# Kernel optimization log

Measured on AMD Instinct MI355X. Metric: run time of the kernel, lower is better.

## Reference

```python
import jax, jax.numpy as jnp
import numpy as np

TOP_K = 2

def setup_inputs() -> dict:
    key = jax.random.key(0)
    k1, k2, k3, k4 = jax.random.split(key, 4)
    T, H, E, I = 2048, 1024, 16, 768
    x = jax.random.normal(k1, (T, H), dtype=jnp.float32)
    gate_w = jax.random.normal(k2, (E, H), dtype=jnp.float32) * 0.02
    w13 = jax.random.normal(k3, (E, 2 * I, H), dtype=jnp.float32) * 0.02
    w2 = jax.random.normal(k4, (E, H, I), dtype=jnp.float32) * 0.02
    return {"x": x, "gate_w": gate_w, "w13": w13, "w2": w2}


def reference(x, gate_w, w13, w2):
    # x: [T, H] tokens; gate_w: [E, H]; w13: [E, 2I, H]; w2: [E, H, I]
    T, H = x.shape
    E = gate_w.shape[0]
    I = w2.shape[-1]

    # --- route: gate matmul + softmax top-k router (renormalize=True) ---
    router_logits = x @ gate_w.T                                  # [T, E]
    probs = jax.nn.softmax(router_logits.astype(jnp.float32), axis=-1)
    topk_w, topk_ids = jax.lax.top_k(probs, TOP_K)                # [T, K]
    topk_w = topk_w / jnp.sum(topk_w, axis=-1, keepdims=True)     # renormalize
    topk_w = topk_w.astype(x.dtype)

    # dense combine weights [T, E]: scatter top-k weights back (dispatch/combine)
    dense_gates = jnp.zeros((T, E), dtype=x.dtype)
    dense_gates = dense_gates.at[jnp.arange(T)[:, None], topk_ids].add(topk_w)

    # --- apply sparse experts: SwiGLU FFN per expert, combined by gates ---
    def expert_step(acc, packed):
        w13_e, w2_e, g_e = packed        # [2I,H], [H,I], [T]
        h = x @ w13_e.T                  # [T, 2I]
        act = jax.nn.silu(h[:, :I]) * h[:, I:]   # gate_proj * up_proj
        return acc + g_e[:, None] * (act @ w2_e.T), None

    acc0 = jnp.zeros_like(x)
    out, _ = jax.lax.scan(expert_step, acc0, (w13, w2, dense_gates.T))
    return out
```

## Files before the change

### kernel.cpp

```cpp
#include <hip/hip_runtime.h>
#include <hip/hip_bf16.h>
#include <hip/hip_fp16.h>
#include <math.h>

#define T_TOK 2048
#define HDIM  1024
#define NEXP  16
#define IDIM  768
#define BM    32
#define MAXROWS 4608

using f16   = _Float16;
using f16x4 = __attribute__((ext_vector_type(4))) _Float16;
using f16x8 = __attribute__((ext_vector_type(8))) _Float16;
using f32x4 = __attribute__((ext_vector_type(4))) float;

__global__ __launch_bounds__(256) void router_kernel(
    const float* __restrict__ x, const float* __restrict__ gw,
    int* __restrict__ tok_e, float* __restrict__ tok_w, int* __restrict__ cnt)
{
    int wave = threadIdx.x >> 6;
    int lane = threadIdx.x & 63;
    int t = blockIdx.x * 4 + wave;
    if (t >= T_TOK) return;

    const float* xrow = x + (size_t)t * HDIM;
    float xv[16];
#pragma unroll
    for (int j = 0; j < 16; ++j) xv[j] = xrow[lane + 64 * j];

    float logits[NEXP];
#pragma unroll
    for (int e = 0; e < NEXP; ++e) {
        const float* gr = gw + (size_t)e * HDIM;
        float s = 0.f;
#pragma unroll
        for (int j = 0; j < 16; ++j) s += xv[j] * gr[lane + 64 * j];
#pragma unroll
        for (int o = 32; o > 0; o >>= 1) s += __shfl_xor(s, o, 64);
        logits[e] = s;
    }

    int i1 = 0; float m1 = logits[0];
#pragma unroll
    for (int e = 1; e < NEXP; ++e) if (logits[e] > m1) { m1 = logits[e]; i1 = e; }
    int i2 = -1; float m2 = -3.0e38f;
#pragma unroll
    for (int e = 0; e < NEXP; ++e) if (e != i1 && logits[e] > m2) { m2 = logits[e]; i2 = e; }

    float w1 = 1.f / (1.f + expf(m2 - m1));
    float w2 = 1.f - w1;

    if (lane == 0) {
        tok_e[t * 2 + 0] = i1; tok_e[t * 2 + 1] = i2;
        tok_w[t * 2 + 0] = w1; tok_w[t * 2 + 1] = w2;
        atomicAdd(&cnt[i1], 1);
        atomicAdd(&cnt[i2], 1);
    }
}

__global__ void prefix_kernel(const int* __restrict__ cnt, int* __restrict__ base,
                              int* __restrict__ total)
{
    if (threadIdx.x == 0) {
        int b = 0;
        for (int e = 0; e < NEXP; ++e) {
            base[e] = b;
            b += (cnt[e] + BM - 1) & ~(BM - 1);
        }
        base[NEXP] = b;
        *total = b;
    }
}

__global__ __launch_bounds__(256) void scatter_kernel(
    const int* __restrict__ tok_e, const float* __restrict__ tok_w,
    const int* __restrict__ base, int* __restrict__ cnt2,
    int* __restrict__ rowslot, float* __restrict__ rowgate)
{
    int t = blockIdx.x * 256 + threadIdx.x;
    if (t >= T_TOK) return;
#pragma unroll
    for (int k = 0; k < 2; ++k) {
        int e = tok_e[t * 2 + k];
        int pos = atomicAdd(&cnt2[e], 1);
        int row = base[e] + pos;
        rowslot[row] = t * 2 + k;
        rowgate[row] = tok_w[t * 2 + k];
    }
}

__global__ __launch_bounds__(256) void gemm1_kernel(
    const float* __restrict__ x, const float* __restrict__ w13,
    const int* __restrict__ rowslot, const int* __restrict__ base,
    const int* __restrict__ cnt, const int* __restrict__ total,
    f16* __restrict__ act)
{
    int row0 = blockIdx.x * BM;
    if (row0 >= *total) return;
    int nt = blockIdx.y;

    int e = 0;
#pragma unroll
    for (int i = 1; i < NEXP; ++i) if (base[i] <= row0) e = i;
    int basee = base[e], cnte = cnt[e];

    __shared__ f16  a_sm[32 * 40];
    __shared__ f16  b_sm[128 * 40];
    __shared__ float h_sm[32 * 132];

    int tid = threadIdx.x;

    int ar = tid >> 3, ac = (tid & 7) * 4;
    bool avalid = (row0 + ar - basee) < cnte;
    const float* aptr = x;
    if (avalid) {
        int tok = rowslot[row0 + ar] >> 1;
        aptr = x + (size_t)tok * HDIM + ac;
    }

    int br = tid >> 1, bc = (tid & 1) * 16;
    int wrow = (br < 64) ? (nt * 64 + br) : (IDIM + nt * 64 + (br - 64));
    const float* bptr = w13 + (size_t)e * 2 * IDIM * HDIM + (size_t)wrow * HDIM + bc;

    int wv = tid >> 6, lane = tid & 63, l16 = lane & 15, lk = lane >> 4;
    f32x4 acc[2][2] = {};

    for (int k0 = 0; k0 < HDIM; k0 += 32) {
        __syncthreads();
        float4 av = avalid ? *(const float4*)(aptr + k0) : float4{0.f, 0.f, 0.f, 0.f};
        f16x4 a4; a4[0] = (f16)av.x; a4[1] = (f16)av.y; a4[2] = (f16)av.z; a4[3] = (f16)av.w;
        *(f16x4*)&a_sm[ar * 40 + ac] = a4;
#pragma unroll
        for (int i = 0; i < 4; ++i) {
            float4 bv = *(const float4*)(bptr + k0 + i * 4);
            f16x4 b4; b4[0] = (f16)bv.x; b4[1] = (f16)bv.y; b4[2] = (f16)bv.z; b4[3] = (f16)bv.w;
            *(f16x4*)&b_sm[br * 40 + bc + i * 4] = b4;
        }
        __syncthreads();

        f16x8 af0 = *(const f16x8*)&a_sm[(l16) * 40 + lk * 8];
        f16x8 af1 = *(const f16x8*)&a_sm[(16 + l16) * 40 + lk * 8];
        f16x8 bf0 = *(const f16x8*)&b_sm[(wv * 32 + l16) * 40 + lk * 8];
        f16x8 bf1 = *(const f16x8*)&b_sm[(wv * 32 + 16 + l16) * 40 + lk * 8];
        acc[0][0] = __builtin_amdgcn_mfma_f32_16x16x32_f16(af0, bf0, acc[0][0], 0, 0, 0);
        acc[0][1] = __builtin_amdgcn_mfma_f32_16x16x32_f16(af0, bf1, acc[0][1], 0, 0, 0);
        acc[1][0] = __builtin_amdgcn_mfma_f32_16x16x32_f16(af1, bf0, acc[1][0], 0, 0, 0);
        acc[1][1] = __builtin_amdgcn_mfma_f32_16x16x32_f16(af1, bf1, acc[1][1], 0, 0, 0);
    }

    __syncthreads();
#pragma unroll
    for (int mh = 0; mh < 2; ++mh)
#pragma unroll
        for (int nh = 0; nh < 2; ++nh)
#pragma unroll
            for (int j = 0; j < 4; ++j)
                h_sm[(mh * 16 + lk * 4 + j) * 132 + wv * 32 + nh * 16 + l16] = acc[mh][nh][j];
    __syncthreads();

    int rr = tid >> 3, cc = (tid & 7) * 8;
    f16x8 o;
#pragma unroll
    for (int i = 0; i < 8; ++i) {
        float hg = h_sm[rr * 132 + cc + i];
        float hu = h_sm[rr * 132 + 64 + cc + i];
        float s = hg / (1.f + expf(-hg));
        o[i] = (f16)(s * hu);
    }
    *(f16x8*)&act[(size_t)(row0 + rr) * IDIM + nt * 64 + cc] = o;
}

__global__ __launch_bounds__(256) void gemm2_kernel(
    const f16* __restrict__ act, const float* __restrict__ w2,
    const int* __restrict__ rowslot, const float* __restrict__ rowgate,
    const int* __restrict__ base, const int* __restrict__ cnt, const int* __restrict__ total,
    float* __restrict__ out)
{
    int row0 = blockIdx.x * BM;
    if (row0 >= *total) return;
    int nt = blockIdx.y;

    int e = 0;
#pragma unroll
    for (int i = 1; i < NEXP; ++i) if (base[i] <= row0) e = i;
    int basee = base[e], cnte = cnt[e];

    __shared__ f16 a_sm[32 * 40];
    __shared__ f16 b_sm[128 * 40];

    int tid = threadIdx.x;
    int ar = tid >> 3, ac = (tid & 7) * 4;
    const f16* aptr = act + (size_t)(row0 + ar) * IDIM + ac;
    int br = tid >> 1, bc = (tid & 1) * 16;
    const float* bptr = w2 + (size_t)e * HDIM * IDIM + (size_t)(nt * 128 + br) * IDIM + bc;

    int wv = tid >> 6, lane = tid & 63, l16 = lane & 15, lk = lane >> 4;
    f32x4 acc[2][2] = {};

    for (int k0 = 0; k0 < IDIM; k0 += 32) {
        __syncthreads();
        *(f16x4*)&a_sm[ar * 40 + ac] = *(const f16x4*)(aptr + k0);
#pragma unroll
        for (int i = 0; i < 4; ++i) {
            float4 bv = *(const float4*)(bptr + k0 + i * 4);
            f16x4 b4; b4[0] = (f16)bv.x; b4[1] = (f16)bv.y; b4[2] = (f16)bv.z; b4[3] = (f16)bv.w;
            *(f16x4*)&b_sm[br * 40 + bc + i * 4] = b4;
        }
        __syncthreads();

        f16x8 af0 = *(const f16x8*)&a_sm[(l16) * 40 + lk * 8];
        f16x8 af1 = *(const f16x8*)&a_sm[(16 + l16) * 40 + lk * 8];
        f16x8 bf0 = *(const f16x8*)&b_sm[(wv * 32 + l16) * 40 + lk * 8];
        f16x8 bf1 = *(const f16x8*)&b_sm[(wv * 32 + 16 + l16) * 40 + lk * 8];
        acc[0][0] = __builtin_amdgcn_mfma_f32_16x16x32_f16(af0, bf0, acc[0][0], 0, 0, 0);
        acc[0][1] = __builtin_amdgcn_mfma_f32_16x16x32_f16(af0, bf1, acc[0][1], 0, 0, 0);
        acc[1][0] = __builtin_amdgcn_mfma_f32_16x16x32_f16(af1, bf0, acc[1][0], 0, 0, 0);
        acc[1][1] = __builtin_amdgcn_mfma_f32_16x16x32_f16(af1, bf1, acc[1][1], 0, 0, 0);
    }

    int colbase = nt * 128 + wv * 32;
#pragma unroll
    for (int mh = 0; mh < 2; ++mh) {
#pragma unroll
        for (int j = 0; j < 4; ++j) {
            int r = mh * 16 + lk * 4 + j;
            int row = row0 + r;
            if ((row - basee) < cnte) {
                int s = rowslot[row];
                float g = rowgate[row];
                float* orow = out + (size_t)(s >> 1) * HDIM + colbase;
                atomicAdd(&orow[l16], g * acc[mh][0][j]);
                atomicAdd(&orow[16 + l16], g * acc[mh][1][j]);
            }
        }
    }
}

extern "C" void kernel_launch(void* const* d_in, const int* in_sizes, int n_in,
                              void* d_out, int out_size, void* d_ws, size_t ws_size,
                              hipStream_t stream) {
    const float* x   = (const float*)d_in[0];
    const float* gw  = (const float*)d_in[1];
    const float* w13 = (const float*)d_in[2];
    const float* w2  = (const float*)d_in[3];
    float* out = (float*)d_out;

    char* ws = (char*)d_ws;
    size_t off = 0;
    f16* act       = (f16*)(ws + off);   off += (size_t)MAXROWS * IDIM * 2;
    int* rowslot   = (int*)(ws + off);   off += (size_t)MAXROWS * 4;
    float* rowgate = (float*)(ws + off); off += (size_t)MAXROWS * 4;
    int* tok_e     = (int*)(ws + off);   off += (size_t)T_TOK * 2 * 4;
    float* tok_w   = (float*)(ws + off); off += (size_t)T_TOK * 2 * 4;
    int* cnt       = (int*)(ws + off);   off += 64;
    int* cnt2      = (int*)(ws + off);   off += 64;
    int* base      = (int*)(ws + off);   off += 128;
    int* total     = (int*)(ws + off);   off += 64;

    hipMemsetAsync(cnt, 0, 128, stream);
    hipMemsetAsync(out, 0, (size_t)T_TOK * HDIM * 4, stream);

    router_kernel<<<T_TOK / 4, 256, 0, stream>>>(x, gw, tok_e, tok_w, cnt);
    prefix_kernel<<<1, 64, 0, stream>>>(cnt, base, total);
    scatter_kernel<<<T_TOK / 256, 256, 0, stream>>>(tok_e, tok_w, base, cnt2, rowslot, rowgate);

    dim3 g1(MAXROWS / BM, (2 * IDIM) / 128);
    gemm1_kernel<<<g1, 256, 0, stream>>>(x, w13, rowslot, base, cnt, total, act);

    dim3 g2(MAXROWS / BM, HDIM / 128);
    gemm2_kernel<<<g2, 256, 0, stream>>>(act, w2, rowslot, rowgate, base, cnt, total, out);
}
```

Before: 420.8 us.

## Enlarge MoE GEMM row tiles to 128 and fuse SwiGLU from registers

Row tile per block grows from 32 to 128 so each block reuses a 128x32 weight slice across four times more token rows, cutting redundant fp32 weight reads and conversions. Each wave now computes a 32x128 output sub-tile with 16 MFMAs per k-step instead of 4. In gemm1 the shared-memory staging for the SwiGLU epilogue is dropped and the activation is computed directly from accumulators, since gate and up columns sit in the same lane. Larger padding (MAXROWS raised) adds wasted rows per expert, and higher register use may lower occupancy.

Measured after the change: 353.3 us. 16.0% less time.

```diff
diff --git a/kernel.cpp b/kernel.cpp
--- a/kernel.cpp
+++ b/kernel.cpp
@@ -7,13 +7,20 @@
 #define HDIM  1024
 #define NEXP  16
 #define IDIM  768
-#define BM    32
-#define MAXROWS 4608
+#define BM    128
+#define MAXROWS 6144
 
 using f16   = _Float16;
 using f16x4 = __attribute__((ext_vector_type(4))) _Float16;
 using f16x8 = __attribute__((ext_vector_type(8))) _Float16;
 using f32x4 = __attribute__((ext_vector_type(4))) float;
+
+__device__ __forceinline__ f16x8 cvt2(float4 a, float4 b) {
+    f16x8 r;
+    r[0] = (f16)a.x; r[1] = (f16)a.y; r[2] = (f16)a.z; r[3] = (f16)a.w;
+    r[4] = (f16)b.x; r[5] = (f16)b.y; r[6] = (f16)b.z; r[7] = (f16)b.w;
+    return r;
+}
 
 __global__ __launch_bounds__(256) void router_kernel(
     const float* __restrict__ x, const float* __restrict__ gw,
@@ -105,70 +112,73 @@
     for (int i = 1; i < NEXP; ++i) if (base[i] <= row0) e = i;
     int basee = base[e], cnte = cnt[e];
 
-    __shared__ f16  a_sm[32 * 40];
-    __shared__ f16  b_sm[128 * 40];
-    __shared__ float h_sm[32 * 132];
+    __shared__ f16 a_sm[128 * 40];
+    __shared__ f16 b_sm[128 * 40];
 
     int tid = threadIdx.x;
-
-    int ar = tid >> 3, ac = (tid & 7) * 4;
-    bool avalid = (row0 + ar - basee) < cnte;
+    int srow = tid >> 1;
+    int scol = (tid & 1) * 16;
+
+    bool avalid = (unsigned)(row0 + srow - basee) < (unsigned)cnte;
     const float* aptr = x;
     if (avalid) {
-        int tok = rowslot[row0 + ar] >> 1;
-        aptr = x + (size_t)tok * HDIM + ac;
-    }
-
-    int br = tid >> 1, bc = (tid & 1) * 16;
-    int wrow = (br < 64) ? (nt * 64 + br) : (IDIM + nt * 64 + (br - 64));
-    const float* bptr = w13 + (size_t)e * 2 * IDIM * HDIM + (size_t)wrow * HDIM + bc;
+        int tok = rowslot[row0 + srow] >> 1;
+        aptr = x + (size_t)tok * HDIM + scol;
+    }
+
+    int wrow = (srow < 64) ? (nt * 64 + srow) : (IDIM + nt * 64 + (srow - 64));
+    const float* bptr = w13 + (size_t)e * 2 * IDIM * HDIM + (size_t)wrow * HDIM + scol;
 
     int wv = tid >> 6, lane = tid & 63, l16 = lane & 15, lk = lane >> 4;
-    f32x4 acc[2][2] = {};
+    f32x4 acc[2][8] = {};
 
     for (int k0 = 0; k0 < HDIM; k0 += 32) {
         __syncthreads();
-        float4 av = avalid ? *(const float4*)(aptr + k0) : float4{0.f, 0.f, 0.f, 0.f};
-        f16x4 a4; a4[0] = (f16)av.x; a4[1] = (f16)av.y; a4[2] = (f16)av.z; a4[3] = (f16)av.w;
-        *(f16x4*)&a_sm[ar * 40 + ac] = a4;
-#pragma unroll
-        for (int i = 0; i < 4; ++i) {
-            float4 bv = *(const float4*)(bptr + k0 + i * 4);
-            f16x4 b4; b4[0] = (f16)bv.x; b4[1] = (f16)bv.y; b4[2] = (f16)bv.z; b4[3] = (f16)bv.w;
-            *(f16x4*)&b_sm[br * 40 + bc + i * 4] = b4;
-        }
-        __syncthreads();
-
-        f16x8 af0 = *(const f16x8*)&a_sm[(l16) * 40 + lk * 8];
-        f16x8 af1 = *(const f16x8*)&a_sm[(16 + l16) * 40 + lk * 8];
-        f16x8 bf0 = *(const f16x8*)&b_sm[(wv * 32 + l16) * 40 + lk * 8];
-        f16x8 bf1 = *(const f16x8*)&b_sm[(wv * 32 + 16 + l16) * 40 + lk * 8];
-        acc[0][0] = __builtin_amdgcn_mfma_f32_16x16x32_f16(af0, bf0, acc[0][0], 0, 0, 0);
-        acc[0][1] = __builtin_amdgcn_mfma_f32_16x16x32_f16(af0, bf1, acc[0][1], 0, 0, 0);
-        acc[1][0] = __builtin_amdgcn_mfma_f32_16x16x32_f16(af1, bf0, acc[1][0], 0, 0, 0);
-        acc[1][1] = __builtin_amdgcn_mfma_f32_16x16x32_f16(af1, bf1, acc[1][1], 0, 0, 0);
-    }
-
-    __syncthreads();
-#pragma unroll
-    for (int mh = 0; mh < 2; ++mh)
-#pragma unroll
-        for (int nh = 0; nh < 2; ++nh)
-#pragma unroll
-            for (int j = 0; j < 4; ++j)
-                h_sm[(mh * 16 + lk * 4 + j) * 132 + wv * 32 + nh * 16 + l16] = acc[mh][nh][j];
-    __syncthreads();
-
-    int rr = tid >> 3, cc = (tid & 7) * 8;
-    f16x8 o;
-#pragma unroll
-    for (int i = 0; i < 8; ++i) {
-        float hg = h_sm[rr * 132 + cc + i];
-        float hu = h_sm[rr * 132 + 64 + cc + i];
-        float s = hg / (1.f + expf(-hg));
-        o[i] = (f16)(s * hu);
-    }
-    *(f16x8*)&act[(size_t)(row0 + rr) * IDIM + nt * 64 + cc] = o;
+        {
+            float4 a0{0,0,0,0}, a1{0,0,0,0}, a2{0,0,0,0}, a3{0,0,0,0};
+            if (avalid) {
+                a0 = *(const float4*)(aptr + k0);
+                a1 = *(const float4*)(aptr + k0 + 4);
+                a2 = *(const float4*)(aptr + k0 + 8);
+                a3 = *(const float4*)(aptr + k0 + 12);
+            }
+            float4 b0 = *(const float4*)(bptr + k0);
+            float4 b1 = *(const float4*)(bptr + k0 + 4);
+            float4 b2 = *(const float4*)(bptr + k0 + 8);
+            float4 b3 = *(const float4*)(bptr + k0 + 12);
+            *(f16x8*)&a_sm[srow * 40 + scol]     = cvt2(a0, a1);
+            *(f16x8*)&a_sm[srow * 40 + scol + 8] = cvt2(a2, a3);
+            *(f16x8*)&b_sm[srow * 40 + scol]     = cvt2(b0, b1);
+            *(f16x8*)&b_sm[srow * 40 + scol + 8] = cvt2(b2, b3);
+        }
+        __syncthreads();
+
+        f16x8 af[2], bf[8];
+#pragma unroll
+        for (int m = 0; m < 2; ++m)
+            af[m] = *(const f16x8*)&a_sm[(wv * 32 + m * 16 + l16) * 40 + lk * 8];
+#pragma unroll
+        for (int n = 0; n < 8; ++n)
+            bf[n] = *(const f16x8*)&b_sm[(n * 16 + l16) * 40 + lk * 8];
+#pragma unroll
+        for (int m = 0; m < 2; ++m)
+#pragma unroll
+            for (int n = 0; n < 8; ++n)
+                acc[m][n] = __builtin_amdgcn_mfma_f32_16x16x32_f16(af[m], bf[n], acc[m][n], 0, 0, 0);
+    }
+
+#pragma unroll
+    for (int m = 0; m < 2; ++m)
+#pragma unroll
+        for (int n = 0; n < 4; ++n)
+#pragma unroll
+            for (int j = 0; j < 4; ++j) {
+                float hg = acc[m][n][j];
+                float hu = acc[m][n + 4][j];
+                float s = hg / (1.f + expf(-hg));
+                int row = row0 + wv * 32 + m * 16 + lk * 4 + j;
+                act[(size_t)row * IDIM + nt * 64 + n * 16 + l16] = (f16)(s * hu);
+            }
 }
 
 __global__ __launch_bounds__(256) void gemm2_kernel(
@@ -186,55 +196,63 @@
     for (int i = 1; i < NEXP; ++i) if (base[i] <= row0) e = i;
     int basee = base[e], cnte = cnt[e];
 
-    __shared__ f16 a_sm[32 * 40];
+    __shared__ f16 a_sm[128 * 40];
     __shared__ f16 b_sm[128 * 40];
 
     int tid = threadIdx.x;
-    int ar = tid >> 3, ac = (tid & 7) * 4;
-    const f16* aptr = act + (size_t)(row0 + ar) * IDIM + ac;
-    int br = tid >> 1, bc = (tid & 1) * 16;
-    const float* bptr = w2 + (size_t)e * HDIM * IDIM + (size_t)(nt * 128 + br) * IDIM + bc;
+    int srow = tid >> 1;
+    int scol = (tid & 1) * 16;
+
+    const f16*   aptr = act + (size_t)(row0 + srow) * IDIM + scol;
+    const float* bptr = w2 + (size_t)e * HDIM * IDIM + (size_t)(nt * 128 + srow) * IDIM + scol;
 
     int wv = tid >> 6, lane = tid & 63, l16 = lane & 15, lk = lane >> 4;
-    f32x4 acc[2][2] = {};
+    f32x4 acc[2][8] = {};
 
     for (int k0 = 0; k0 < IDIM; k0 += 32) {
         __syncthreads();
-        *(f16x4*)&a_sm[ar * 40 + ac] = *(const f16x4*)(aptr + k0);
-#pragma unroll
-        for (int i = 0; i < 4; ++i) {
-            float4 bv = *(const float4*)(bptr + k0 + i * 4);
-            f16x4 b4; b4[0] = (f16)bv.x; b4[1] = (f16)bv.y; b4[2] = (f16)bv.z; b4[3] = (f16)bv.w;
-            *(f16x4*)&b_sm[br * 40 + bc + i * 4] = b4;
-        }
-        __syncthreads();
-
-        f16x8 af0 = *(const f16x8*)&a_sm[(l16) * 40 + lk * 8];
-        f16x8 af1 = *(const f16x8*)&a_sm[(16 + l16) * 40 + lk * 8];
-        f16x8 bf0 = *(const f16x8*)&b_sm[(wv * 32 + l16) * 40 + lk * 8];
-        f16x8 bf1 = *(const f16x8*)&b_sm[(wv * 32 + 16 + l16) * 40 + lk * 8];
-        acc[0][0] = __builtin_amdgcn_mfma_f32_16x16x32_f16(af0, bf0, acc[0][0], 0, 0, 0);
-        acc[0][1] = __builtin_amdgcn_mfma_f32_16x16x32_f16(af0, bf1, acc[0][1], 0, 0, 0);
-        acc[1][0] = __builtin_amdgcn_mfma_f32_16x16x32_f16(af1, bf0, acc[1][0], 0, 0, 0);
-        acc[1][1] = __builtin_amdgcn_mfma_f32_16x16x32_f16(af1, bf1, acc[1][1], 0, 0, 0);
-    }
-
-    int colbase = nt * 128 + wv * 32;
-#pragma unroll
-    for (int mh = 0; mh < 2; ++mh) {
+        {
+            f16x8 alo = *(const f16x8*)(aptr + k0);
+            f16x8 ahi = *(const f16x8*)(aptr + k0 + 8);
+            float4 b0 = *(const float4*)(bptr + k0);
+            float4 b1 = *(const float4*)(bptr + k0 + 4);
+            float4 b2 = *(const float4*)(bptr + k0 + 8);
+            float4 b3 = *(const float4*)(bptr + k0 + 12);
+            *(f16x8*)&a_sm[srow * 40 + scol]     = alo;
+            *(f16x8*)&a_sm[srow * 40 + scol + 8] = ahi;
+            *(f16x8*)&b_sm[srow * 40 + scol]     = cvt2(b0, b1);
+            *(f16x8*)&b_sm[srow * 40 + scol + 8] = cvt2(b2, b3);
+        }
+        __syncthreads();
+
+        f16x8 af[2], bf[8];
+#pragma unroll
+        for (int m = 0; m < 2; ++m)
+            af[m] = *(const f16x8*)&a_sm[(wv * 32 + m * 16 + l16) * 40 + lk * 8];
+#pragma unroll
+        for (int n = 0; n < 8; ++n)
+            bf[n] = *(const f16x8*)&b_sm[(n * 16 + l16) * 40 + lk * 8];
+#pragma unroll
+        for (int m = 0; m < 2; ++m)
+#pragma unroll
+            for (int n = 0; n < 8; ++n)
+                acc[m][n] = __builtin_amdgcn_mfma_f32_16x16x32_f16(af[m], bf[n], acc[m][n], 0, 0, 0);
+    }
+
+#pragma unroll
+    for (int m = 0; m < 2; ++m)
 #pragma unroll
         for (int j = 0; j < 4; ++j) {
-            int r = mh * 16 + lk * 4 + j;
-            int row = row0 + r;
-            if ((row - basee) < cnte) {
+            int row = row0 + wv * 32 + m * 16 + lk * 4 + j;
+            if ((unsigned)(row - basee) < (unsigned)cnte) {
                 int s = rowslot[row];
                 float g = rowgate[row];
-                float* orow = out + (size_t)(s >> 1) * HDIM + colbase;
-                atomicAdd(&orow[l16], g * acc[mh][0][j]);
-                atomicAdd(&orow[16 + l16], g * acc[mh][1][j]);
+                float* orow = out + (size_t)(s >> 1) * HDIM + nt * 128;
+#pragma unroll
+                for (int n = 0; n < 8; ++n)
+                    atomicAdd(&orow[n * 16 + l16], g * acc[m][n][j]);
             }
         }
-    }
 }
 
 extern "C" void kernel_launch(void* const* d_in, const int* in_sizes, int n_in,
```
